# Kernel tuning notes

Hardware: AMD Instinct MI355X
Metric: run time of the kernel (lower is better)

## Reference

```python
import jax, jax.numpy as jnp
import numpy as np
from jax import lax

TEMPLATE = 21          # template_size
SEARCH = 9             # search_range
PAD = TEMPLATE // 2    # conv padding


def setup_inputs() -> dict:
    key = jax.random.key(0)
    k1, k2 = jax.random.split(key)
    B, H, W = 4, 480, 640
    p1 = jax.random.uniform(k1, (B, 1, H, W), dtype=jnp.float32)
    p2 = jax.random.uniform(k2, (B, 1, H, W), dtype=jnp.float32)
    return {"p1": p1, "p2": p2}


def _box_sum(x):
    # 21x21 box filter (conv with all-ones kernel), same padding, stride 1.
    kernel = jnp.ones((1, 1, TEMPLATE, TEMPLATE), x.dtype)
    return lax.conv_general_dilated(x, kernel, (1, 1), [(PAD, PAD), (PAD, PAD)])


def reference(p1, p2):
    p1 = p1.astype(jnp.float32)
    p2 = p2.astype(jnp.float32)
    B, _, H, W = p1.shape
    R = SEARCH

    # zero-pad search margin around p2
    p2_padded = jnp.pad(p2, ((0, 0), (0, 0), (R, R), (R, R)))

    # (361, 2) offsets, iterated dy-major / dx-minor to match the torch loop order
    dys, dxs = jnp.meshgrid(jnp.arange(-R, R + 1), jnp.arange(-R, R + 1), indexing='ij')
    offsets = jnp.stack([dys.reshape(-1), dxs.reshape(-1)], axis=-1)  # rows: (dy, dx)

    max0 = jnp.full((B, 1, H, W), -1.0, dtype=jnp.float32)
    flow0 = jnp.zeros((B, 2, H, W), dtype=jnp.float32)

    def step(carry, off):
        max_score, flow = carry
        dy, dx = off[0], off[1]
        shifted = lax.dynamic_slice(p2_padded, (0, 0, R + dy, R + dx), (B, 1, H, W))
        agreement = p1 * shifted + (1.0 - p1) * (1.0 - shifted)
        corr = _box_sum(agreement)                  # (B,1,H,W)
        mask = corr > max_score
        max_score = jnp.where(mask, corr, max_score)
        m = mask[:, 0]                               # (B,H,W)
        fx = jnp.where(m, dx.astype(jnp.float32), flow[:, 0])
        fy = jnp.where(m, dy.astype(jnp.float32), flow[:, 1])
        flow = jnp.stack([fx, fy], axis=1)
        return (max_score, flow), None

    (max_score, flow), _ = lax.scan(step, (max0, flow0), offsets)

    particle_density = _box_sum(p1)
    confidence = jnp.clip(particle_density / float(TEMPLATE * TEMPLATE), 0.0, 1.0)
    return flow, confidence
```

## Files before the change

### kernel.cpp

```cpp
#include <hip/hip_runtime.h>


#define HH 480
#define WW 640
#define TH 32
#define TW 32
#define QROWS 52
#define PROWS 70
#define PCOLS 70
#define PSTR  71
#define RSTR  36
#define MARGIN 0.002f
#define NPIX (4 * HH * WW)

__device__ __forceinline__ float replay_corr(const float* __restrict__ p1b,
                                             const float* __restrict__ p2b,
                                             int y, int x, int k) {
  int dy = k / 19 - 9, dx = k % 19 - 9;
  float s = 0.f;
  for (int u = 0; u < 21; ++u) {
    int yy = y - 10 + u;
    if (yy < 0 || yy >= HH) continue;
    int y2 = yy + dy;
    bool yok = (y2 >= 0 && y2 < HH);
    const float* r1 = p1b + yy * WW;
    const float* r2 = p2b + y2 * WW;
#pragma unroll
    for (int v = 0; v < 21; ++v) {
      int xx = x - 10 + v;
      if (xx < 0 || xx >= WW) continue;
      float p = r1[xx];
      int x2 = xx + dx;
      float s2 = (yok && x2 >= 0 && x2 < WW) ? r2[x2] : 0.f;
      float t2 = __fmul_rn(__fsub_rn(1.f, p), __fsub_rn(1.f, s2));
      float agr = __fmaf_rn(p, s2, t2);
      s = __fadd_rn(s, agr);
    }
  }
  return s;
}

__global__ __launch_bounds__(256, 4)
void bcm_pass1(const float* __restrict__ p1, const float* __restrict__ p2,
               float* __restrict__ out, unsigned* __restrict__ wl,
               unsigned capE) {
  __shared__ float ps[PROWS * PSTR];
  __shared__ __align__(16) float rsb0[QROWS * RSTR];
  __shared__ __align__(16) float rsb1[QROWS * RSTR];

  const int tid = threadIdx.x;
  const int b  = blockIdx.z;
  const int y0 = blockIdx.y * TH;
  const int x0 = blockIdx.x * TW;
  const float* p1b = p1 + b * HH * WW;
  const float* p2b = p2 + b * HH * WW;

  for (int i = tid; i < PROWS * PCOLS; i += 256) {
    int rr = i / PCOLS, cc = i - rr * PCOLS;
    int Y = y0 - 19 + rr, X = x0 - 19 + cc;
    float v = 0.f;
    if (Y >= 0 && Y < HH && X >= 0 && X < WW) v = p2b[Y * WW + X];
    ps[rr * PSTR + cc] = v;
  }

  const int col = tid & 31;
  const int r0  = (tid >> 5) * 4;
  const int prow_ = tid >> 2;
  const int c0    = (tid & 3) * 8;
  const bool active1 = (prow_ < QROWS);

  float qreg[28];
  if (active1) {
    int Y = y0 - 10 + prow_;
    bool yok = (Y >= 0 && Y < HH);
    const float* qrow = p1b + Y * WW;
#pragma unroll
    for (int t = 0; t < 28; ++t) {
      int X = x0 - 10 + c0 + t;
      float v = 0.f;
      if (yok && X >= 0 && X < WW) v = 2.f * qrow[X] - 1.f;
      qreg[t] = v;
    }
  }
  __syncthreads();

  float bv[4][4];
  int   bk[4][4];
#pragma unroll
  for (int j = 0; j < 4; ++j)
#pragma unroll
    for (int t = 0; t < 4; ++t) { bv[j][t] = -1e30f; bk[j][t] = 0; }

  float preg[28];
  int k = 0;
  for (int dy = -9; dy <= 9; ++dy) {
    const float* prowp = active1 ? &ps[(prow_ + dy + 9) * PSTR + c0] : ps;
    if (active1) {
#pragma unroll
      for (int t = 0; t < 28; ++t) preg[t] = prowp[t];
    }
#pragma unroll
    for (int dxi = 0; dxi < 19; ++dxi, ++k) {
      float* slab = (k & 1) ? rsb1 : rsb0;
      if (active1) {
        float s = 0.f;
#pragma unroll
        for (int t = 0; t < 21; ++t) s += qreg[t] * preg[(dxi + t) % 28];
        float rs[8];
        rs[0] = s;
#pragma unroll
        for (int j = 1; j < 8; ++j) {
          s += qreg[j + 20] * preg[(dxi + j + 20) % 28]
             - qreg[j - 1] * preg[(dxi + j - 1) % 28];
          rs[j] = s;
        }
        float4* w = (float4*)&slab[prow_ * RSTR + c0];
        w[0] = make_float4(rs[0], rs[1], rs[2], rs[3]);
        w[1] = make_float4(rs[4], rs[5], rs[6], rs[7]);
        if (dxi < 18) preg[dxi % 28] = prowp[dxi + 28];
      }
      __syncthreads();
      {
        float s = 0.f;
#pragma unroll
        for (int u = 0; u < 21; ++u) s += slab[(r0 + u) * RSTR + col];
#pragma unroll
        for (int j = 0; j < 4; ++j) {
          if (j > 0) s += slab[(r0 + 20 + j) * RSTR + col]
                        - slab[(r0 + j - 1) * RSTR + col];
          float cv = s;
          if (cv > bv[j][3]) {
            int ck = k;
#pragma unroll
            for (int t = 0; t < 4; ++t) {
              if (cv > bv[j][t]) {
                float tv = bv[j][t]; int tk = bk[j][t];
                bv[j][t] = cv; bk[j][t] = ck;
                cv = tv; ck = tk;
              }
            }
          }
        }
      }
    }
  }

  __syncthreads();
  if (active1) {
    float s = 0.f;
#pragma unroll
    for (int t = 0; t < 21; ++t) s += qreg[t];
    float rs[8];
    rs[0] = s;
#pragma unroll
    for (int j = 1; j < 8; ++j) {
      s += qreg[j + 20] - qreg[j - 1];
      rs[j] = s;
    }
    float4* w = (float4*)&rsb0[prow_ * RSTR + c0];
    w[0] = make_float4(rs[0], rs[1], rs[2], rs[3]);
    w[1] = make_float4(rs[4], rs[5], rs[6], rs[7]);
  }
  __syncthreads();

  unsigned* cntN = wl;
  unsigned* cntD = wl + 1;
  uint4* entries = (uint4*)(wl + 8);
  const unsigned capHalf = capE >> 1;
  const int confoff = 4 * 2 * HH * WW;
  {
    float s = 0.f;
#pragma unroll
    for (int u = 0; u < 21; ++u) s += rsb0[(r0 + u) * RSTR + col];
#pragma unroll
    for (int j = 0; j < 4; ++j) {
      if (j > 0) s += rsb0[(r0 + 20 + j) * RSTR + col]
                    - rsb0[(r0 + j - 1) * RSTR + col];
      int y = y0 + r0 + j;
      int x = x0 + col;
      int ny = min(y + 10, HH - 1) - max(y - 10, 0) + 1;
      int nx = min(x + 10, WW - 1) - max(x - 10, 0) + 1;
      float c = (s + (float)(ny * nx)) * (1.f / 882.f);
      float conf = fminf(fmaxf(c, 0.f), 1.f);

      int kwin = bk[j][0];
      float ofx = (float)(kwin % 19 - 9);
      float ofy = (float)(kwin / 19 - 9);

      if (bv[j][0] - bv[j][1] <= MARGIN) {
        int cand[4];
        int n = 1; cand[0] = bk[j][0];
#pragma unroll
        for (int t = 1; t < 4; ++t)
          if (bv[j][0] - bv[j][t] <= MARGIN) cand[n++] = bk[j][t];
        bool deep = (bv[j][0] - bv[j][3] <= MARGIN);
        unsigned pix = (unsigned)((b * HH + y) * WW + x);
        bool stored = false;
        if (!deep) {
          unsigned slot = atomicAdd(cntN, 1u);
          if (slot < capHalf) {
            unsigned kk[4];
#pragma unroll
            for (int t = 0; t < 4; ++t)
              kk[t] = (t < n) ? (unsigned)cand[t] : 0xFFFFu;
            uint4 e;
            e.x = pix;
            e.y = kk[0] | (kk[1] << 16);
            e.z = kk[2] | (kk[3] << 16);
            e.w = 0u;
            entries[slot] = e;
            stored = true;
          }
        } else {
          unsigned ds = atomicAdd(cntD, 1u);
          if (ds < capHalf) {
            uint4 e; e.x = pix; e.y = 0u; e.z = 0u; e.w = 0u;
            entries[capE - 1 - ds] = e;
            stored = true;
          }
        }
        if (!stored) {
          int c2 = (n > 2) ? cand[2] : cand[0];
          int c3 = (n > 3) ? cand[3] : cand[0];
          int dpf = deep ? 1 : 0;
          ofx = (float)(1000000 + cand[0] + 512 * cand[1]);
          ofy = (float)(c2 + 512 * c3 + 262144 * dpf);
        }
      }
      out[((b * 2 + 0) * HH + y) * WW + x] = ofx;
      out[((b * 2 + 1) * HH + y) * WW + x] = ofy;
      out[confoff + (b * HH + y) * WW + x] = conf;
    }
  }
}

__global__ __launch_bounds__(256)
void bcm_pass2(const float* __restrict__ p1, const float* __restrict__ p2,
               float* __restrict__ out, const unsigned* __restrict__ wl,
               unsigned capE) {
  const unsigned capHalf = capE >> 1;
  unsigned rawN = wl[0], rawD = wl[1];
  unsigned nN = rawN > capHalf ? capHalf : rawN;
  unsigned nD = rawD > capHalf ? capHalf : rawD;
  const uint4* entries = (const uint4*)(wl + 8);
  const int lane = threadIdx.x & 63;
  unsigned wid = blockIdx.x * (blockDim.x >> 6) + (threadIdx.x >> 6);
  unsigned nw = gridDim.x * (blockDim.x >> 6);

  for (unsigned base = wid * 16; base < nN; base += nw * 16) {
    unsigned e = base + (lane >> 2);
    int c = lane & 3;
    float wv = -1e30f;
    int   wk = 0x7FFF;
    unsigned pix = 0;
    bool valid = (e < nN);
    if (valid) {
      uint4 ent = entries[e];
      pix = ent.x;
      unsigned kc = (c == 0) ? (ent.y & 0xFFFFu) :
                    (c == 1) ? (ent.y >> 16) :
                    (c == 2) ? (ent.z & 0xFFFFu) : (ent.z >> 16);
      if (kc != 0xFFFFu) {
        int b = pix / (HH * WW);
        int r = pix - b * (HH * WW);
        int y = r / WW, x = r - y * WW;
        wv = replay_corr(p1 + b * HH * WW, p2 + b * HH * WW, y, x, (int)kc);
        wk = (int)kc;
      }
    }
#pragma unroll
    for (int d = 1; d <= 2; d <<= 1) {
      float ov = __shfl_xor(wv, d, 64);
      int   ok = __shfl_xor(wk, d, 64);
      if (ov > wv || (ov == wv && ok < wk)) { wv = ov; wk = ok; }
    }
    if (valid && c == 0) {
      int b = pix / (HH * WW);
      int r = pix - b * (HH * WW);
      int y = r / WW, x = r - y * WW;
      int fxi = (b * 2 * HH + y) * WW + x;
      out[fxi] = (float)(wk % 19 - 9);
      out[fxi + HH * WW] = (float)(wk / 19 - 9);
    }
  }

  for (unsigned d = wid; d < nD; d += nw) {
    uint4 ent = entries[capE - 1 - d];
    unsigned pix = ent.x;
    int b = pix / (HH * WW);
    int r = pix - b * (HH * WW);
    int y = r / WW, x = r - y * WW;
    const float* p1b = p1 + b * HH * WW;
    const float* p2b = p2 + b * HH * WW;
    float wv = -1e30f;
    int   wk = 0x7FFF;
    for (int k = lane; k < 361; k += 64) {
      float s = replay_corr(p1b, p2b, y, x, k);
      if (s > wv || (s == wv && k < wk)) { wv = s; wk = k; }
    }
    for (int off = 32; off > 0; off >>= 1) {
      float ov = __shfl_down(wv, off, 64);
      int   ok = __shfl_down(wk, off, 64);
      if (ov > wv || (ov == wv && ok < wk)) { wv = ov; wk = ok; }
    }
    if (lane == 0) {
      int fxi = (b * 2 * HH + y) * WW + x;
      out[fxi] = (float)(wk % 19 - 9);
      out[fxi + HH * WW] = (float)(wk / 19 - 9);
    }
  }

  if (rawN > capHalf || rawD > capHalf) {
    int stride = gridDim.x * blockDim.x;
    for (int idx = blockIdx.x * blockDim.x + threadIdx.x; idx < NPIX;
         idx += stride) {
      int b = idx / (HH * WW);
      int r = idx - b * (HH * WW);
      int fxi = b * 2 * HH * WW + r;
      float fx = out[fxi];
      if (fx < 500000.f) continue;
      int fyi = fxi + HH * WW;
      int p = (int)fx - 1000000;
      int q = (int)out[fyi];
      int deep = q >> 18;
      int kk[4] = {p & 511, p >> 9, q & 511, (q >> 9) & 511};
      int y = r / WW, x = r - y * WW;
      const float* p1b = p1 + b * HH * WW;
      const float* p2b = p2 + b * HH * WW;
      float wv = 0.f; int win = -1;
      if (deep) {
        for (int k = 0; k < 361; ++k) {
          float s = replay_corr(p1b, p2b, y, x, k);
          if (win < 0 || s > wv) { wv = s; win = k; }
        }
      } else {
        for (int c = 0; c < 4; ++c) {
          int k = kk[c];
          float s = replay_corr(p1b, p2b, y, x, k);
          if (win < 0 || s > wv || (s == wv && k < win)) { wv = s; win = k; }
        }
      }
      out[fxi] = (float)(win % 19 - 9);
      out[fyi] = (float)(win / 19 - 9);
    }
  }
}

extern "C" void kernel_launch(void* const* d_in, const int* in_sizes, int n_in,
                              void* d_out, int out_size, void* d_ws, size_t ws_size,
                              hipStream_t stream) {
  const float* p1 = (const float*)d_in[0];
  const float* p2 = (const float*)d_in[1];
  float* out = (float*)d_out;
  unsigned* wl = (unsigned*)d_ws;
  unsigned capE = (ws_size >= 64) ? (unsigned)((ws_size - 32) / 16) : 0u;
  hipMemsetAsync(d_ws, 0, 32, stream);
  dim3 grid1(WW / TW, HH / TH, 4);
  bcm_pass1<<<grid1, dim3(256), 0, stream>>>(p1, p2, out, wl, capE);
  bcm_pass2<<<dim3(512), dim3(256), 0, stream>>>(p1, p2, out, wl, capE);
}
```

Before: 717.4 us.

## Transpose row-sum slab with XOR swizzle and halve vertical-pass threads

Row sums are now stored transposed (column-major) in a swizzled shared buffer, so the vertical 21-tap pass reads float4 runs and computes 8 outputs per thread with a prefix-difference sliding window. Only 128 threads do this pass. The top-4 insertion becomes a branchless select network, with the indices packed as 16-bit pairs. The aim is to cut LDS traffic and bank conflicts in the per-shift vertical sum. The cost is more registers (launch bounds drop to 3 blocks per CU) and idle threads during the vertical pass.

```diff
diff --git a/kernel.cpp b/kernel.cpp
--- a/kernel.cpp
+++ b/kernel.cpp
@@ -9,9 +9,16 @@
 #define PROWS 70
 #define PCOLS 70
 #define PSTR  71
-#define RSTR  36
+#define CSTR  64
 #define MARGIN 0.002f
 #define NPIX (4 * HH * WW)
+
+__device__ __forceinline__ int sw_g(int c) {
+  return (c & 7) ^ (((c >> 3) & 3) << 1);
+}
+__device__ __forceinline__ int swadr(int c, int r) {
+  return c * CSTR + ((((r >> 2) ^ sw_g(c)) << 2) | (r & 3));
+}
 
 __device__ __forceinline__ float replay_corr(const float* __restrict__ p1b,
                                              const float* __restrict__ p2b,
@@ -40,13 +47,12 @@
   return s;
 }
 
-__global__ __launch_bounds__(256, 4)
+__global__ __launch_bounds__(256, 3)
 void bcm_pass1(const float* __restrict__ p1, const float* __restrict__ p2,
                float* __restrict__ out, unsigned* __restrict__ wl,
                unsigned capE) {
   __shared__ float ps[PROWS * PSTR];
-  __shared__ __align__(16) float rsb0[QROWS * RSTR];
-  __shared__ __align__(16) float rsb1[QROWS * RSTR];
+  __shared__ __align__(16) float rsbT[2][32 * CSTR];
 
   const int tid = threadIdx.x;
   const int b  = blockIdx.z;
@@ -64,10 +70,25 @@
   }
 
   const int col = tid & 31;
-  const int r0  = (tid >> 5) * 4;
+  const int rg  = (tid >> 5) & 3;
+  const int r0c = rg * 8;
+  const bool active2 = (tid < 128);
+
   const int prow_ = tid >> 2;
   const int c0    = (tid & 3) * 8;
   const bool active1 = (prow_ < QROWS);
+
+  int roff[7];
+  {
+    const int g  = sw_g(col);
+    const int rb = r0c >> 2;
+#pragma unroll
+    for (int m = 0; m < 7; ++m)
+      roff[m] = col * CSTR + (((rb + m) ^ g) << 2);
+  }
+  int woff[8];
+#pragma unroll
+  for (int j = 0; j < 8; ++j) woff[j] = swadr(c0 + j, prow_);
 
   float qreg[28];
   if (active1) {
@@ -84,12 +105,14 @@
   }
   __syncthreads();
 
-  float bv[4][4];
-  int   bk[4][4];
-#pragma unroll
-  for (int j = 0; j < 4; ++j)
-#pragma unroll
-    for (int t = 0; t < 4; ++t) { bv[j][t] = -1e30f; bk[j][t] = 0; }
+  float    bv[8][4];
+  unsigned bkp[8][2];
+#pragma unroll
+  for (int i = 0; i < 8; ++i) {
+#pragma unroll
+    for (int t = 0; t < 4; ++t) bv[i][t] = -1e30f;
+    bkp[i][0] = 0u; bkp[i][1] = 0u;
+  }
 
   float preg[28];
   int k = 0;
@@ -101,7 +124,7 @@
     }
 #pragma unroll
     for (int dxi = 0; dxi < 19; ++dxi, ++k) {
-      float* slab = (k & 1) ? rsb1 : rsb0;
+      float* slab = rsbT[k & 1];
       if (active1) {
         float s = 0.f;
 #pragma unroll
@@ -114,29 +137,43 @@
              - qreg[j - 1] * preg[(dxi + j - 1) % 28];
           rs[j] = s;
         }
-        float4* w = (float4*)&slab[prow_ * RSTR + c0];
-        w[0] = make_float4(rs[0], rs[1], rs[2], rs[3]);
-        w[1] = make_float4(rs[4], rs[5], rs[6], rs[7]);
+#pragma unroll
+        for (int j = 0; j < 8; ++j) slab[woff[j]] = rs[j];
         if (dxi < 18) preg[dxi % 28] = prowp[dxi + 28];
       }
       __syncthreads();
-      {
-        float s = 0.f;
-#pragma unroll
-        for (int u = 0; u < 21; ++u) s += slab[(r0 + u) * RSTR + col];
-#pragma unroll
-        for (int j = 0; j < 4; ++j) {
-          if (j > 0) s += slab[(r0 + 20 + j) * RSTR + col]
-                        - slab[(r0 + j - 1) * RSTR + col];
-          float cv = s;
-          if (cv > bv[j][3]) {
-            int ck = k;
-#pragma unroll
-            for (int t = 0; t < 4; ++t) {
-              if (cv > bv[j][t]) {
-                float tv = bv[j][t]; int tk = bk[j][t];
-                bv[j][t] = cv; bk[j][t] = ck;
-                cv = tv; ck = tk;
+      if (active2) {
+        const unsigned ck = (unsigned)k;
+        float acc = 0.f, pfx[8];
+#pragma unroll
+        for (int m = 0; m < 7; ++m) {
+          const float4 v = *(const float4*)&slab[roff[m]];
+          const float vv[4] = {v.x, v.y, v.z, v.w};
+#pragma unroll
+          for (int q = 0; q < 4; ++q) {
+            const int u = m * 4 + q;
+            if (u < 8) pfx[u] = acc;
+            acc += vv[q];
+            if (u >= 20) {
+              const int i = u - 20;
+              const float cv = acc - pfx[i];
+              if (cv > bv[i][3]) {
+                const bool g0 = cv > bv[i][0];
+                const bool g1 = cv > bv[i][1];
+                const bool g2 = cv > bv[i][2];
+                bv[i][3] = g2 ? bv[i][2] : cv;
+                bv[i][2] = g2 ? (g1 ? bv[i][1] : cv) : bv[i][2];
+                bv[i][1] = g1 ? (g0 ? bv[i][0] : cv) : bv[i][1];
+                bv[i][0] = g0 ? cv : bv[i][0];
+                const unsigned lo = bkp[i][0], hi = bkp[i][1];
+                const unsigned k0 = lo & 0xFFFFu, k1 = lo >> 16;
+                const unsigned k2 = hi & 0xFFFFu;
+                const unsigned k3n = g2 ? k2 : ck;
+                const unsigned k2n = g2 ? (g1 ? k1 : ck) : k2;
+                const unsigned k1n = g1 ? (g0 ? k0 : ck) : k1;
+                const unsigned k0n = g0 ? ck : k0;
+                bkp[i][0] = k0n | (k1n << 16);
+                bkp[i][1] = k2n | (k3n << 16);
               }
             }
           }
@@ -157,9 +194,8 @@
       s += qreg[j + 20] - qreg[j - 1];
       rs[j] = s;
     }
-    float4* w = (float4*)&rsb0[prow_ * RSTR + c0];
-    w[0] = make_float4(rs[0], rs[1], rs[2], rs[3]);
-    w[1] = make_float4(rs[4], rs[5], rs[6], rs[7]);
+#pragma unroll
+    for (int j = 0; j < 8; ++j) rsbT[0][woff[j]] = rs[j];
   }
   __syncthreads();
 
@@ -168,32 +204,46 @@
   uint4* entries = (uint4*)(wl + 8);
   const unsigned capHalf = capE >> 1;
   const int confoff = 4 * 2 * HH * WW;
-  {
-    float s = 0.f;
-#pragma unroll
-    for (int u = 0; u < 21; ++u) s += rsb0[(r0 + u) * RSTR + col];
-#pragma unroll
-    for (int j = 0; j < 4; ++j) {
-      if (j > 0) s += rsb0[(r0 + 20 + j) * RSTR + col]
-                    - rsb0[(r0 + j - 1) * RSTR + col];
-      int y = y0 + r0 + j;
+  if (active2) {
+    float o[8];
+    {
+      float acc = 0.f, pfx[8];
+#pragma unroll
+      for (int m = 0; m < 7; ++m) {
+        const float4 v = *(const float4*)&rsbT[0][roff[m]];
+        const float vv[4] = {v.x, v.y, v.z, v.w};
+#pragma unroll
+        for (int q = 0; q < 4; ++q) {
+          const int u = m * 4 + q;
+          if (u < 8) pfx[u] = acc;
+          acc += vv[q];
+          if (u >= 20) o[u - 20] = acc - pfx[u - 20];
+        }
+      }
+    }
+#pragma unroll
+    for (int i = 0; i < 8; ++i) {
+      int y = y0 + r0c + i;
       int x = x0 + col;
       int ny = min(y + 10, HH - 1) - max(y - 10, 0) + 1;
       int nx = min(x + 10, WW - 1) - max(x - 10, 0) + 1;
-      float c = (s + (float)(ny * nx)) * (1.f / 882.f);
+      float c = (o[i] + (float)(ny * nx)) * (1.f / 882.f);
       float conf = fminf(fmaxf(c, 0.f), 1.f);
 
-      int kwin = bk[j][0];
-      float ofx = (float)(kwin % 19 - 9);
-      float ofy = (float)(kwin / 19 - 9);
-
-      if (bv[j][0] - bv[j][1] <= MARGIN) {
+      int kk0 = (int)(bkp[i][0] & 0xFFFFu);
+      int kk1 = (int)(bkp[i][0] >> 16);
+      int kk2 = (int)(bkp[i][1] & 0xFFFFu);
+      int kk3 = (int)(bkp[i][1] >> 16);
+      float ofx = (float)(kk0 % 19 - 9);
+      float ofy = (float)(kk0 / 19 - 9);
+
+      if (bv[i][0] - bv[i][1] <= MARGIN) {
         int cand[4];
-        int n = 1; cand[0] = bk[j][0];
-#pragma unroll
-        for (int t = 1; t < 4; ++t)
-          if (bv[j][0] - bv[j][t] <= MARGIN) cand[n++] = bk[j][t];
-        bool deep = (bv[j][0] - bv[j][3] <= MARGIN);
+        int n = 1; cand[0] = kk0;
+        cand[n++] = kk1;
+        if (bv[i][0] - bv[i][2] <= MARGIN) cand[n++] = kk2;
+        if (bv[i][0] - bv[i][3] <= MARGIN) cand[n++] = kk3;
+        bool deep = (bv[i][0] - bv[i][3] <= MARGIN);
         unsigned pix = (unsigned)((b * HH + y) * WW + x);
         bool stored = false;
         if (!deep) {
```

Result: slower. 874.9 us (+22.0%).
